# Performance work log

Hardware: AMD Instinct MI355X
Metric: run time of the kernel (lower is better)

Reference implementation:

```python
import jax, jax.numpy as jnp
import numpy as np

N_SAMPLES = 50000
B = 128
C, H, W = 3, 32, 32
N_CLASSES = 10


def setup_inputs() -> dict:
    key = jax.random.key(0)
    k1, k2, k3 = jax.random.split(key, 3)
    input_batch = jax.random.normal(k1, (B, C, H, W), dtype=jnp.float32)
    samples = jax.random.normal(k2, (N_SAMPLES, C, H, W), dtype=jnp.float32)
    classes = jax.random.randint(k3, (N_SAMPLES,), 0, N_CLASSES, dtype=jnp.int64)
    return {"input_batch": input_batch, "samples": samples, "classes": classes,
            "n_classes": N_CLASSES}


def reference(input_batch, samples, classes, n_classes):
    bs = input_batch.shape[0]
    n = samples.shape[0]
    x = input_batch.reshape(bs, -1)          # (B, D)
    s = samples.reshape(n, -1)               # (N, D)
    x2 = jnp.sum(x * x, axis=1, keepdims=True)           # (B, 1)
    s2 = jnp.sum(s * s, axis=1)[None, :]                 # (1, N)
    d2 = x2 + s2 - 2.0 * jnp.einsum('bd,nd->bn', x, s)   # (B, N)
    dists = jnp.sqrt(jnp.maximum(d2, 0.0))               # L2 distance
    l2s = jnp.min(dists, axis=1)                          # (B,)
    best = jnp.argmin(dists, axis=1)                      # (B,) indices into samples
    pred = jnp.zeros((bs, n_classes), dtype=jnp.float32)
    pred = pred.at[jnp.arange(bs), classes[best]].set(1.0)
    imgs = samples[best]                                  # (B, C, H, W)
    return pred, imgs, l2s
```

## Files before the change

### kernel.cpp

```cpp
#include <hip/hip_runtime.h>
#include <math.h>

#define D      3072
#define BK     64
#define NCH    (D / BK)
#define BM     128
#define NQ     128
#define NCLS   10

typedef float   f32x4  __attribute__((ext_vector_type(4)));
typedef float   f32x16 __attribute__((ext_vector_type(16)));
typedef __bf16  bf16x8 __attribute__((ext_vector_type(8)));

#define WS_GMIN 0
#define WS_X2   1024
#define WS_XHI  4096
#define WS_XLO  (4096 + NCH * 16384)

__global__ __launch_bounds__(64) void prep_kernel(const float* __restrict__ x,
                                                  char* __restrict__ ws) {
    const int q = blockIdx.x;
    const int l = threadIdx.x;
    unsigned long long* gmin = (unsigned long long*)(ws + WS_GMIN);
    float* x2g = (float*)(ws + WS_X2);
    unsigned short* xhi = (unsigned short*)(ws + WS_XHI);
    unsigned short* xlo = (unsigned short*)(ws + WS_XLO);

    const float* xr = x + (size_t)q * D;
    const int swz = (q & 7) << 3;
    float v2 = 0.f;
    for (int c = 0; c < NCH; ++c) {
        float v = xr[c * 64 + l];
        v2 += v * v;
        __bf16 hb = (__bf16)v;
        float  hf = (float)hb;
        __bf16 lb = (__bf16)(v - hf);
        const int idx = c * 8192 + ((q * 64 + l) ^ swz);
        xhi[idx] = __builtin_bit_cast(unsigned short, hb);
        xlo[idx] = __builtin_bit_cast(unsigned short, lb);
    }
#pragma unroll
    for (int off = 32; off > 0; off >>= 1) v2 += __shfl_down(v2, off, 64);
    if (l == 0) { x2g[q] = v2; gmin[q] = ~0ull; }
}

__global__ __launch_bounds__(256, 2) void dist_kernel(const float* __restrict__ s,
                                                      char* __restrict__ ws,
                                                      int N) {
    __shared__ __align__(16) char pool[65536];
    unsigned short* Ahi = (unsigned short*)(pool);
    unsigned short* Alo = (unsigned short*)(pool + 16384);
    unsigned short* Bhi = (unsigned short*)(pool + 32768);
    unsigned short* Blo = (unsigned short*)(pool + 49152);
    float (*s2p)[16]            = (float (*)[16])(pool + 32768);
    float* s2loc                = (float*)(pool + 32768 + 8192);
    unsigned long long (*qmin2)[NQ] =
        (unsigned long long (*)[NQ])(pool + 32768 + 8192 + 512);

    const int tid   = threadIdx.x;
    const int nbase = blockIdx.x * BM;
    const float* x2g = (const float*)(ws + WS_X2);
    unsigned long long* gmin = (unsigned long long*)(ws + WS_GMIN);

    const int c4 = tid & 15;
    const int r0 = tid >> 4;
    const float* gs[8];
    int   wofs[8];
    float s2a[8];
#pragma unroll
    for (int i = 0; i < 8; ++i) {
        const int r = i * 16 + r0;
        int g = nbase + r; if (g > N - 1) g = N - 1;
        gs[i]   = s + (size_t)g * D + c4 * 4;
        wofs[i] = (r * 64 + c4 * 4) ^ ((r & 7) << 3);
        s2a[i]  = 0.f;
    }

    const int lane = tid & 63;
    const int w    = tid >> 6;
    const int wr   = w >> 1;
    const int wc   = w & 1;
    const int l31  = lane & 31;
    const int lhi  = lane >> 5;
    int aBase[2], aMask[2], bBase[2], bMask[2];
#pragma unroll
    for (int i = 0; i < 2; ++i) {
        const int row = wr * 64 + i * 32 + l31;
        aBase[i] = row * 64 + lhi * 8;
        aMask[i] = (row & 7) << 3;
        const int col = wc * 64 + i * 32 + l31;
        bBase[i] = col * 64 + lhi * 8;
        bMask[i] = (col & 7) << 3;
    }

    f32x16 acc[2][2] = {};

    const char* xhiB = ws + WS_XHI;
    const char* xloB = ws + WS_XLO;

    for (int c = 0; c < NCH; ++c) {
        {
            const char* gh = xhiB + (size_t)c * 16384 + tid * 16;
            const char* gl = xloB + (size_t)c * 16384 + tid * 16;
            char* lh = (char*)Bhi + tid * 16;
            char* ll = (char*)Blo + tid * 16;
#pragma unroll
            for (int u = 0; u < 4; ++u) {
                __builtin_amdgcn_global_load_lds(
                    (__attribute__((address_space(1))) void*)(gh + u * 4096),
                    (__attribute__((address_space(3))) void*)(lh + u * 4096), 16, 0, 0);
                __builtin_amdgcn_global_load_lds(
                    (__attribute__((address_space(1))) void*)(gl + u * 4096),
                    (__attribute__((address_space(3))) void*)(ll + u * 4096), 16, 0, 0);
            }
        }
        f32x4 t[8];
#pragma unroll
        for (int i = 0; i < 8; ++i) t[i] = *(const f32x4*)(gs[i] + (size_t)c * 64);
#pragma unroll
        for (int i = 0; i < 8; ++i) {
            unsigned short h[4], lo[4];
#pragma unroll
            for (int e = 0; e < 4; ++e) {
                float v = t[i][e];
                __bf16 hb = (__bf16)v;
                float  hf = (float)hb;
                __bf16 lb = (__bf16)(v - hf);
                h[e]  = __builtin_bit_cast(unsigned short, hb);
                lo[e] = __builtin_bit_cast(unsigned short, lb);
                s2a[i] = fmaf(v, v, s2a[i]);
            }
            uint2 hp, lp;
            hp.x = (unsigned)h[0]  | ((unsigned)h[1]  << 16);
            hp.y = (unsigned)h[2]  | ((unsigned)h[3]  << 16);
            lp.x = (unsigned)lo[0] | ((unsigned)lo[1] << 16);
            lp.y = (unsigned)lo[2] | ((unsigned)lo[3] << 16);
            *(uint2*)&Ahi[wofs[i]] = hp;
            *(uint2*)&Alo[wofs[i]] = lp;
        }
        __syncthreads();

#pragma unroll
        for (int ks = 0; ks < 4; ++ks) {
            bf16x8 a_h[2], a_l[2], b_h[2], b_l[2];
#pragma unroll
            for (int i = 0; i < 2; ++i) {
                a_h[i] = *(const bf16x8*)&Ahi[(aBase[i] + ks * 16) ^ aMask[i]];
                a_l[i] = *(const bf16x8*)&Alo[(aBase[i] + ks * 16) ^ aMask[i]];
                b_h[i] = *(const bf16x8*)&Bhi[(bBase[i] + ks * 16) ^ bMask[i]];
                b_l[i] = *(const bf16x8*)&Blo[(bBase[i] + ks * 16) ^ bMask[i]];
            }
#pragma unroll
            for (int i = 0; i < 2; ++i)
#pragma unroll
                for (int j = 0; j < 2; ++j) {
                    acc[i][j] = __builtin_amdgcn_mfma_f32_32x32x16_bf16(a_h[i], b_h[j], acc[i][j], 0, 0, 0);
                    acc[i][j] = __builtin_amdgcn_mfma_f32_32x32x16_bf16(a_h[i], b_l[j], acc[i][j], 0, 0, 0);
                    acc[i][j] = __builtin_amdgcn_mfma_f32_32x32x16_bf16(a_l[i], b_h[j], acc[i][j], 0, 0, 0);
                }
        }
        __syncthreads();
    }

#pragma unroll
    for (int i = 0; i < 8; ++i) s2p[i * 16 + r0][c4] = s2a[i];
    __syncthreads();
    if (tid < BM) {
        float t2 = 0.f;
#pragma unroll
        for (int j2 = 0; j2 < 16; ++j2) t2 += s2p[tid][j2];
        s2loc[tid] = t2;
    }
    __syncthreads();

#pragma unroll
    for (int j = 0; j < 2; ++j) {
        const int q = wc * 64 + j * 32 + l31;
        const float x2q = x2g[q];
        unsigned long long m = ~0ull;
#pragma unroll
        for (int i = 0; i < 2; ++i) {
#pragma unroll
            for (int r = 0; r < 16; ++r) {
                const int rl = wr * 64 + i * 32 + (r & 3) + 8 * (r >> 2) + 4 * lhi;
                const int n  = nbase + rl;
                if (n < N) {
                    float d2 = fmaxf(x2q + s2loc[rl] - 2.f * acc[i][j][r], 0.f);
                    unsigned long long p =
                        ((unsigned long long)__float_as_uint(d2) << 32) | (unsigned)n;
                    m = p < m ? p : m;
                }
            }
        }
        unsigned long long o = __shfl_xor(m, 32, 64);
        m = o < m ? o : m;
        if (lane < 32) qmin2[wr][q] = m;
    }
    __syncthreads();
    if (tid < NQ) {
        unsigned long long m = qmin2[0][tid];
        unsigned long long o = qmin2[1][tid];
        m = o < m ? o : m;
        atomicMin(&gmin[tid], m);
    }
}

__global__ __launch_bounds__(256) void out_kernel(const float* __restrict__ x,
                                                  const float* __restrict__ s,
                                                  const int* __restrict__ classes,
                                                  const char* __restrict__ ws,
                                                  float* __restrict__ out, int B_) {
    const int b = blockIdx.x;
    const int tid = threadIdx.x;
    const unsigned long long* gmin = (const unsigned long long*)(ws + WS_GMIN);
    const unsigned idx = (unsigned)(gmin[b] & 0xffffffffu);

    float* pred = out;
    float* imgs = out + (size_t)B_ * NCLS;
    float* l2s  = out + (size_t)B_ * NCLS + (size_t)B_ * D;

    if (tid < NCLS) {
        const int cls = classes[idx];
        pred[b * NCLS + tid] = (tid == cls) ? 1.f : 0.f;
    }

    const f32x4* xs4 = (const f32x4*)(x + (size_t)b * D);
    const f32x4* sr4 = (const f32x4*)(s + (size_t)idx * D);
    f32x4* dst = (f32x4*)(imgs + (size_t)b * D);
    float part = 0.f;
    for (int t = tid; t < D / 4; t += 256) {
        f32x4 sv = sr4[t];
        f32x4 xv = xs4[t];
        dst[t] = sv;
        f32x4 d = xv - sv;
        part += d[0] * d[0] + d[1] * d[1] + d[2] * d[2] + d[3] * d[3];
    }
    __shared__ float wsum[4];
#pragma unroll
    for (int off = 32; off > 0; off >>= 1) part += __shfl_down(part, off, 64);
    if ((tid & 63) == 0) wsum[tid >> 6] = part;
    __syncthreads();
    if (tid == 0) l2s[b] = sqrtf(wsum[0] + wsum[1] + wsum[2] + wsum[3]);
}

extern "C" void kernel_launch(void* const* d_in, const int* in_sizes, int n_in,
                              void* d_out, int out_size, void* d_ws, size_t ws_size,
                              hipStream_t stream) {
    const float* x       = (const float*)d_in[0];
    const float* s       = (const float*)d_in[1];
    const int*   classes = (const int*)d_in[2];
    const int B_ = in_sizes[0] / D;
    const int N  = in_sizes[2];
    char* ws = (char*)d_ws;

    prep_kernel<<<B_, 64, 0, stream>>>(x, ws);

    const int nblocks = (N + BM - 1) / BM;
    dist_kernel<<<nblocks, 256, 0, stream>>>(s, ws, N);

    out_kernel<<<B_, 256, 0, stream>>>(x, s, classes, ws, (float*)d_out, B_);
}
```

Before: 847.8 us.

## Prefetch next sample chunk into registers during MFMA and widen prep kernel

The distance kernel now issues the global loads for the next K-chunk of samples before the MFMA loop of the current chunk, using explicit waitcnt and s_barrier with sched_barriers so the loads overlap compute. The aim is to hide global memory latency of the sample reads behind the matrix work. The prep kernel is also rewritten to use 256 threads with vectorized float4 loads and packed stores. This raises register pressure in the main kernel and relies on hand-counted vmcnt values being correct.

```diff
diff --git a/kernel.cpp b/kernel.cpp
--- a/kernel.cpp
+++ b/kernel.cpp
@@ -17,10 +17,10 @@
 #define WS_XHI  4096
 #define WS_XLO  (4096 + NCH * 16384)
 
-__global__ __launch_bounds__(64) void prep_kernel(const float* __restrict__ x,
-                                                  char* __restrict__ ws) {
-    const int q = blockIdx.x;
-    const int l = threadIdx.x;
+__global__ __launch_bounds__(256) void prep_kernel(const float* __restrict__ x,
+                                                   char* __restrict__ ws) {
+    const int q   = blockIdx.x;
+    const int tid = threadIdx.x;
     unsigned long long* gmin = (unsigned long long*)(ws + WS_GMIN);
     float* x2g = (float*)(ws + WS_X2);
     unsigned short* xhi = (unsigned short*)(ws + WS_XHI);
@@ -29,19 +29,41 @@
     const float* xr = x + (size_t)q * D;
     const int swz = (q & 7) << 3;
     float v2 = 0.f;
-    for (int c = 0; c < NCH; ++c) {
-        float v = xr[c * 64 + l];
-        v2 += v * v;
-        __bf16 hb = (__bf16)v;
-        float  hf = (float)hb;
-        __bf16 lb = (__bf16)(v - hf);
-        const int idx = c * 8192 + ((q * 64 + l) ^ swz);
-        xhi[idx] = __builtin_bit_cast(unsigned short, hb);
-        xlo[idx] = __builtin_bit_cast(unsigned short, lb);
+#pragma unroll
+    for (int i = 0; i < 3; ++i) {
+        const int f  = tid + i * 256;
+        const int c  = f >> 4;
+        const int l4 = (f & 15) * 4;
+        f32x4 v = *(const f32x4*)(xr + f * 4);
+        unsigned short h[4], lo[4];
+#pragma unroll
+        for (int e = 0; e < 4; ++e) {
+            float val = v[e];
+            v2 = fmaf(val, val, v2);
+            __bf16 hb = (__bf16)val;
+            float  hf = (float)hb;
+            __bf16 lb = (__bf16)(val - hf);
+            h[e]  = __builtin_bit_cast(unsigned short, hb);
+            lo[e] = __builtin_bit_cast(unsigned short, lb);
+        }
+        const int idx = c * 8192 + ((q * 64 + l4) ^ swz);
+        uint2 hp, lp;
+        hp.x = (unsigned)h[0]  | ((unsigned)h[1]  << 16);
+        hp.y = (unsigned)h[2]  | ((unsigned)h[3]  << 16);
+        lp.x = (unsigned)lo[0] | ((unsigned)lo[1] << 16);
+        lp.y = (unsigned)lo[2] | ((unsigned)lo[3] << 16);
+        *(uint2*)&xhi[idx] = hp;
+        *(uint2*)&xlo[idx] = lp;
     }
 #pragma unroll
     for (int off = 32; off > 0; off >>= 1) v2 += __shfl_down(v2, off, 64);
-    if (l == 0) { x2g[q] = v2; gmin[q] = ~0ull; }
+    __shared__ float wsum[4];
+    if ((tid & 63) == 0) wsum[tid >> 6] = v2;
+    __syncthreads();
+    if (tid == 0) {
+        x2g[q] = wsum[0] + wsum[1] + wsum[2] + wsum[3];
+        gmin[q] = ~0ull;
+    }
 }
 
 __global__ __launch_bounds__(256, 2) void dist_kernel(const float* __restrict__ s,
@@ -98,6 +120,10 @@
     const char* xhiB = ws + WS_XHI;
     const char* xloB = ws + WS_XLO;
 
+    f32x4 t[8];
+#pragma unroll
+    for (int i = 0; i < 8; ++i) t[i] = *(const f32x4*)(gs[i]);
+
     for (int c = 0; c < NCH; ++c) {
         {
             const char* gh = xhiB + (size_t)c * 16384 + tid * 16;
@@ -114,9 +140,8 @@
                     (__attribute__((address_space(3))) void*)(ll + u * 4096), 16, 0, 0);
             }
         }
-        f32x4 t[8];
-#pragma unroll
-        for (int i = 0; i < 8; ++i) t[i] = *(const f32x4*)(gs[i] + (size_t)c * 64);
+        __builtin_amdgcn_sched_barrier(0);
+
 #pragma unroll
         for (int i = 0; i < 8; ++i) {
             unsigned short h[4], lo[4];
@@ -138,7 +163,23 @@
             *(uint2*)&Ahi[wofs[i]] = hp;
             *(uint2*)&Alo[wofs[i]] = lp;
         }
-        __syncthreads();
+        __builtin_amdgcn_sched_barrier(0);
+
+        if (c + 1 < NCH) {
+#pragma unroll
+            for (int i = 0; i < 8; ++i)
+                t[i] = *(const f32x4*)(gs[i] + (size_t)(c + 1) * 64);
+        }
+        __builtin_amdgcn_sched_barrier(0);
+
+        if (c + 1 < NCH) {
+            asm volatile("s_waitcnt vmcnt(8) lgkmcnt(0)" ::: "memory");
+        } else {
+            asm volatile("s_waitcnt vmcnt(0) lgkmcnt(0)" ::: "memory");
+        }
+        __builtin_amdgcn_sched_barrier(0);
+        __builtin_amdgcn_s_barrier();
+        __builtin_amdgcn_sched_barrier(0);
 
 #pragma unroll
         for (int ks = 0; ks < 4; ++ks) {
@@ -159,7 +200,8 @@
                     acc[i][j] = __builtin_amdgcn_mfma_f32_32x32x16_bf16(a_l[i], b_h[j], acc[i][j], 0, 0, 0);
                 }
         }
-        __syncthreads();
+        __builtin_amdgcn_s_barrier();
+        __builtin_amdgcn_sched_barrier(0);
     }
 
 #pragma unroll
@@ -253,7 +295,7 @@
     const int N  = in_sizes[2];
     char* ws = (char*)d_ws;
 
-    prep_kernel<<<B_, 64, 0, stream>>>(x, ws);
+    prep_kernel<<<B_, 256, 0, stream>>>(x, ws);
 
     const int nblocks = (N + BM - 1) / BM;
     dist_kernel<<<nblocks, 256, 0, stream>>>(s, ws, N);
```

After: 833.9 us. Within noise of the previous version (-1.6%).
